# Kernel tuning notes

Hardware: AMD Instinct MI355X
Metric: run time of the kernel (lower is better)

Reference implementation:

```python
import math
import jax, jax.numpy as jnp
import numpy as np

B, T, D = 2, 2048, 1024
NUM_HEADS = 16
NUM_KV_HEADS = 4
HEAD_DIM = 64
ROPE_THETA = 500000.0


def precompute_freqs_cis(dim, seq_len, theta):
    freqs = 1.0 / theta ** (jnp.arange(0, dim, 2).astype(jnp.float32) / dim)
    freqs = jnp.outer(jnp.arange(seq_len), freqs)  # [T, dim//2]
    return jnp.cos(freqs), jnp.sin(freqs)


def apply_rotary_emb(xq, xk, cos, sin):
    # xq:[B,T,H,Dh], cos/sin:[T,Dh//2] -> broadcast as [1,T,1,Dh//2]
    c = cos[None, :, None, :]
    s = sin[None, :, None, :]

    def rot(x):
        xr = x.reshape(*x.shape[:-1], -1, 2)
        x0, x1 = xr[..., 0], xr[..., 1]
        return jnp.stack([x0 * c - x1 * s, x1 * c + x0 * s], axis=-1).reshape(x.shape)

    return rot(xq), rot(xk)


def setup_inputs() -> dict:
    key = jax.random.key(0)
    ks = jax.random.split(key, 5)
    x = jax.random.normal(ks[0], (B, T, D), dtype=jnp.float32)
    # causal mask [B,1,T,T]
    mask = jnp.broadcast_to(jnp.tril(jnp.ones((T, T), dtype=bool))[None, None], (B, 1, T, T))
    sq = 1.0 / math.sqrt(D)
    Wq = jax.random.normal(ks[1], (D, NUM_HEADS * HEAD_DIM), dtype=jnp.float32) * sq
    Wk = jax.random.normal(ks[2], (D, NUM_KV_HEADS * HEAD_DIM), dtype=jnp.float32) * sq
    Wv = jax.random.normal(ks[3], (D, NUM_KV_HEADS * HEAD_DIM), dtype=jnp.float32) * sq
    Wo = jax.random.normal(ks[4], (NUM_HEADS * HEAD_DIM, D), dtype=jnp.float32) * (1.0 / math.sqrt(NUM_HEADS * HEAD_DIM))
    return {"x": x, "mask": mask, "Wq": Wq, "Wk": Wk, "Wv": Wv, "Wo": Wo}


def reference(x, mask, Wq, Wk, Wv, Wo):
    b, t, _ = x.shape
    n_rep = NUM_HEADS // NUM_KV_HEADS
    q = (x @ Wq).reshape(b, t, NUM_HEADS, HEAD_DIM)
    k = (x @ Wk).reshape(b, t, NUM_KV_HEADS, HEAD_DIM)
    v = (x @ Wv).reshape(b, t, NUM_KV_HEADS, HEAD_DIM)
    cos, sin = precompute_freqs_cis(HEAD_DIM, t, ROPE_THETA)
    q, k = apply_rotary_emb(q, k, cos, sin)
    k = jnp.repeat(k, n_rep, axis=2)
    v = jnp.repeat(v, n_rep, axis=2)
    q = q.transpose(0, 2, 1, 3)  # [B,H,T,Dh]
    k = k.transpose(0, 2, 1, 3)
    v = v.transpose(0, 2, 1, 3)
    scale = 1.0 / math.sqrt(HEAD_DIM)
    attn = jnp.einsum('bhqd,bhkd->bhqk', q, k) * scale
    attn = jnp.where(mask, attn, -1e9)
    attn = jax.nn.softmax(attn, axis=-1)
    out = jnp.einsum('bhqk,bhkd->bhqd', attn, v)
    out = out.transpose(0, 2, 1, 3).reshape(b, t, -1)
    return out @ Wo
```

## Files before the change

### kernel.cpp

```cpp
#include <hip/hip_runtime.h>
#include <hip/hip_bf16.h>

#define B_  2
#define T_  2048
#define D_  1024
#define H_  16
#define KH_ 4
#define DH_ 64

typedef __attribute__((ext_vector_type(8))) short bf16x8;
typedef __attribute__((ext_vector_type(4))) float f32x4;

#define QSCALE 0.18033688011112043f

#if defined(__has_builtin)
#  if __has_builtin(__builtin_amdgcn_exp2f)
#    define EXP2F(x) __builtin_amdgcn_exp2f(x)
#  endif
#endif
#ifndef EXP2F
#  define EXP2F(x) exp2f(x)
#endif

__device__ __forceinline__ unsigned short f2bf(float f) {
  union { float f; unsigned int u; } v; v.f = f;
  return (unsigned short)((v.u + 0x7FFFu + ((v.u >> 16) & 1u)) >> 16);
}
__device__ __forceinline__ unsigned int pk2(float a, float b) {
  union { __hip_bfloat162 h2; unsigned int u; } v;
  v.h2 = __float22bfloat162_rn(make_float2(a, b));
  return v.u;
}

__device__ __forceinline__ void g2l16(const void* g, void* l) {
  __builtin_amdgcn_global_load_lds(
      (const __attribute__((address_space(1))) void*)g,
      (__attribute__((address_space(3))) void*)l, 16, 0, 0);
}


__global__ __launch_bounds__(256) void prep_kernel(
    const float* __restrict__ x,  const float* __restrict__ Wq,
    const float* __restrict__ Wk, const float* __restrict__ Wv,
    const float* __restrict__ Wo,
    short* __restrict__ xb, short* __restrict__ WT, short* __restrict__ WoT,
    float2* __restrict__ tbl) {
  __shared__ short Ts[64 * 72];
  const int bid = blockIdx.x, tid = threadIdx.x;

  if (bid < 2048) {
    const size_t i8 = ((size_t)bid * 256 + tid) * 8;
    const float4 a = *(const float4*)&x[i8];
    const float4 b = *(const float4*)&x[i8 + 4];
    uint4 p; p.x = pk2(a.x, a.y); p.y = pk2(a.z, a.w);
    p.z = pk2(b.x, b.y); p.w = pk2(b.z, b.w);
    *(uint4*)&xb[i8] = p;
  } else if (bid < 2688) {
    const bool isW = bid < 2432;
    const int idx = isW ? (bid - 2048) : (bid - 2432);
    const int n0 = (idx >> 4) * 64, k0 = (idx & 15) * 64;
    const float* src; int ncols, c0; short* dst;
    if (isW) {
      dst = WT;
      if (n0 < 1024)      { src = Wq; ncols = 1024; c0 = n0; }
      else if (n0 < 1280) { src = Wk; ncols = 256;  c0 = n0 - 1024; }
      else                { src = Wv; ncols = 256;  c0 = n0 - 1280; }
    } else { dst = WoT; src = Wo; ncols = 1024; c0 = n0; }
    for (int i = tid; i < 1024; i += 256) {
      const int kr = i >> 4, c4 = (i & 15) << 2;
      const int kc = isW ? kr : ((kr & 15) * 4 + (kr >> 4));
      const float4 w = *(const float4*)&src[(size_t)(k0 + kr) * ncols + c0 + c4];
      Ts[(c4 + 0) * 72 + kc] = (short)f2bf(w.x);
      Ts[(c4 + 1) * 72 + kc] = (short)f2bf(w.y);
      Ts[(c4 + 2) * 72 + kc] = (short)f2bf(w.z);
      Ts[(c4 + 3) * 72 + kc] = (short)f2bf(w.w);
    }
    __syncthreads();
    for (int c = tid; c < 512; c += 256) {
      const int nr = c >> 3, c8 = (c & 7) * 8;
      *(bf16x8*)&dst[(size_t)(n0 + nr) * 1024 + k0 + c8] =
          *(const bf16x8*)&Ts[nr * 72 + c8];
    }
  } else {
    const int e = (bid - 2688) * 256 + tid;
    const int t = e >> 5, i2 = e & 31;
    const float freq = exp2f(-(float)(2 * i2) * (18.931568569324174f / 64.0f));
    float sn, cs; sincosf((float)t * freq, &sn, &cs);
    tbl[e] = make_float2(cs, sn);
  }
}

__global__ __launch_bounds__(256) void qkv_mfma_kernel(
    const short* __restrict__ xb, const short* __restrict__ WT,
    const float2* __restrict__ tbl,
    short* __restrict__ qo, short* __restrict__ ko, short* __restrict__ vt) {
  __shared__ short Xs[128 * 128];
  __shared__ short Wt[64 * 128];
  const int tid = threadIdx.x;
  const int lane = tid & 63, w = tid >> 6;
  const int lm = lane & 15, quad = lane >> 4;
  const int lr = lane >> 4;
  const int lb = lane & 15;
  const int m0 = blockIdx.x * 128;
  const int n0 = blockIdx.y * 64;

  f32x4 acc[2][4];
  #pragma unroll
  for (int sm = 0; sm < 2; ++sm)
    #pragma unroll
    for (int ct = 0; ct < 4; ++ct) acc[sm][ct] = (f32x4){0.f, 0.f, 0.f, 0.f};

  for (int kt = 0; kt < 8; ++kt) {
    __syncthreads();
    #pragma unroll
    for (int u = 0; u < 8; ++u) {
      const int r = (w * 8 + u) * 4 + lr;
      const int sb = lb ^ (r & 7);
      g2l16(&xb[(size_t)(m0 + r) * 1024 + kt * 128 + sb * 8],
            &Xs[(w * 8 + u) * 512]);
    }
    #pragma unroll
    for (int u = 0; u < 4; ++u) {
      const int r = (w * 4 + u) * 4 + lr;
      const int sb = lb ^ (r & 7);
      g2l16(&WT[(size_t)(n0 + r) * 1024 + kt * 128 + sb * 8],
            &Wt[(w * 4 + u) * 512]);
    }
    asm volatile("s_waitcnt vmcnt(0)" ::: "memory");
    __syncthreads();
    #pragma unroll
    for (int s = 0; s < 4; ++s) {
      bf16x8 bfr[4];
      #pragma unroll
      for (int ct = 0; ct < 4; ++ct)
        bfr[ct] = *(const bf16x8*)&Wt[(ct * 16 + lm) * 128 +
                                      (((s * 4 + quad) ^ (lm & 7)) << 3)];
      #pragma unroll
      for (int sm = 0; sm < 2; ++sm) {
        const bf16x8 a = *(const bf16x8*)&Xs[(w * 32 + sm * 16 + lm) * 128 +
                                             (((s * 4 + quad) ^ (lm & 7)) << 3)];
        #pragma unroll
        for (int ct = 0; ct < 4; ++ct)
          acc[sm][ct] =
              __builtin_amdgcn_mfma_f32_16x16x32_bf16(a, bfr[ct], acc[sm][ct], 0, 0, 0);
      }
    }
  }

  if (n0 < 1280) {
    const bool isQ = n0 < 1024;
    short* outp = isQ ? qo : ko;
    const int base = isQ ? n0 : n0 - 1024;
    const int nh = isQ ? H_ : KH_;
    const int hh = base >> 6;
    const float post = isQ ? QSCALE : 1.0f;
    #pragma unroll
    for (int sm = 0; sm < 2; ++sm)
      #pragma unroll
      for (int r = 0; r < 4; ++r) {
        const int row = m0 + w * 32 + sm * 16 + quad * 4 + r;
        const int b = row >> 11, t = row & 2047;
        float v4[4];
        #pragma unroll
        for (int ct = 0; ct < 4; ++ct) {
          float val = acc[sm][ct][r];
          const float other = __shfl_xor(val, 1);
          const int ci = ct * 16 + lm;
          const float2 cs = tbl[t * 32 + (ci >> 1)];
          val = ((ci & 1) == 0) ? (val * cs.x - other * cs.y)
                                : (val * cs.x + other * cs.y);
          v4[ct] = val * post;
        }
        uint2 st; st.x = pk2(v4[0], v4[1]); st.y = pk2(v4[2], v4[3]);
        *(uint2*)&outp[((size_t)(b * nh + hh) * T_ + t) * DH_ + lm * 4] = st;
      }
  } else {
    __syncthreads();
    #pragma unroll
    for (int sm = 0; sm < 2; ++sm)
      #pragma unroll
      for (int r = 0; r < 4; ++r)
        #pragma unroll
        for (int ct = 0; ct < 4; ++ct)
          Xs[(w * 32 + sm * 16 + quad * 4 + r) * 72 + ct * 16 + lm] =
              (short)f2bf(acc[sm][ct][r]);
    __syncthreads();
    const int kh = (n0 - 1280) >> 6;
    const int b = m0 >> 11, t0 = m0 & 2047;
    short* vb = vt + (size_t)(b * KH_ + kh) * DH_ * T_;
    for (int c = tid; c < 1024; c += 256) {
      const int d = c >> 4, c8 = (c & 15) * 8;
      short tmp[8];
      #pragma unroll
      for (int j = 0; j < 8; ++j) {
        const int s = c8 + j, sg = s & 63;
        const int tok = (s & 64) + ((sg & 3) << 4) + (sg >> 2);
        tmp[j] = Xs[tok * 72 + d];
      }
      *(bf16x8*)&vb[(size_t)d * T_ + t0 + c8] = *(bf16x8*)tmp;
    }
  }
}

__global__ __launch_bounds__(256) void attn_mfma_kernel(
    const short* __restrict__ q, const short* __restrict__ k,
    const short* __restrict__ vt, short* __restrict__ att) {
  __shared__ short Ks[128 * 72];
  __shared__ short Vts[64 * 136];
  __shared__ short Ps0[64 * 72];
  __shared__ short Ps1[64 * 72];

  const int bx = blockIdx.x;
  const int qt = 31 - (bx >> 5);
  const int hb = bx & 31;
  const int h = hb >> 1, b = hb & 1;
  const int kh = h >> 2;
  const int tid = threadIdx.x;
  const int lane = tid & 63, w = tid >> 6;
  const int lm = lane & 15, quad = lane >> 4;
  const int q0 = qt * 64;

  const short* qb = q + (size_t)(b * H_ + h) * T_ * DH_;
  const short* kb = k + (size_t)(b * KH_ + kh) * T_ * DH_;
  const short* vb = vt + (size_t)(b * KH_ + kh) * DH_ * T_;

  bf16x8 ones;
  #pragma unroll
  for (int i = 0; i < 8; ++i) ones[i] = (short)0x3F80;

  bf16x8 aq[2];
  #pragma unroll
  for (int s = 0; s < 2; ++s)
    aq[s] = *(const bf16x8*)&qb[(size_t)(q0 + w * 16 + lm) * 64 + s * 32 + quad * 8];

  bf16x8 pk[4], pv[4];
  #pragma unroll
  for (int u = 0; u < 4; ++u) {
    const int c = tid + u * 256;
    const int row = c >> 3, c8 = (c & 7) * 8;
    pk[u] = *(const bf16x8*)&kb[(size_t)row * 64 + c8];
    const int d = c >> 4, c16 = (c & 15) * 8;
    pv[u] = *(const bf16x8*)&vb[(size_t)d * T_ + c16];
  }

  f32x4 oacc[4], lacc;
  #pragma unroll
  for (int i = 0; i < 4; ++i) oacc[i] = (f32x4){0.f, 0.f, 0.f, 0.f};
  lacc = (f32x4){0.f, 0.f, 0.f, 0.f};

  auto step = [&](int j, bool diag, short* Ps) {
    f32x4 sacc[4];
    #pragma unroll
    for (int i = 0; i < 4; ++i) sacc[i] = (f32x4){0.f, 0.f, 0.f, 0.f};
    __builtin_amdgcn_s_setprio(1);
    #pragma unroll
    for (int s = 0; s < 2; ++s) {
      #pragma unroll
      for (int ct = 0; ct < 4; ++ct) {
        const bf16x8 bb =
            *(const bf16x8*)&Ks[(j * 64 + ct * 16 + lm) * 72 + s * 32 + quad * 8];
        sacc[ct] = __builtin_amdgcn_mfma_f32_16x16x32_bf16(aq[s], bb, sacc[ct], 0, 0, 0);
      }
    }
    __builtin_amdgcn_s_setprio(0);
    if (diag) {
      #pragma unroll
      for (int r = 0; r < 4; ++r) {
        const int qi = w * 16 + quad * 4 + r;
        float p[4];
        #pragma unroll
        for (int ct = 0; ct < 4; ++ct) {
          float pv2 = EXP2F(sacc[ct][r]);
          if ((ct * 16 + lm) > qi) pv2 = 0.f;
          p[ct] = pv2;
        }
        uint2 pw2; pw2.x = pk2(p[0], p[1]); pw2.y = pk2(p[2], p[3]);
        *(uint2*)&Ps[qi * 72 + lm * 4] = pw2;
      }
    } else {
      #pragma unroll
      for (int r = 0; r < 4; ++r) {
        const int qi = w * 16 + quad * 4 + r;
        uint2 pw2;
        pw2.x = pk2(EXP2F(sacc[0][r]), EXP2F(sacc[1][r]));
        pw2.y = pk2(EXP2F(sacc[2][r]), EXP2F(sacc[3][r]));
        *(uint2*)&Ps[qi * 72 + lm * 4] = pw2;
      }
    }
    __builtin_amdgcn_s_setprio(1);
    #pragma unroll
    for (int s = 0; s < 2; ++s) {
      const bf16x8 pa = *(const bf16x8*)&Ps[(w * 16 + lm) * 72 + s * 32 + quad * 8];
      lacc = __builtin_amdgcn_mfma_f32_16x16x32_bf16(pa, ones, lacc, 0, 0, 0);
      #pragma unroll
      for (int ct = 0; ct < 4; ++ct) {
        const bf16x8 vfr = *(const bf16x8*)&Vts[(ct * 16 + lm) * 136 +
                                                j * 64 + s * 32 + quad * 8];
        oacc[ct] = __builtin_amdgcn_mfma_f32_16x16x32_bf16(pa, vfr, oacc[ct], 0, 0, 0);
      }
    }
    __builtin_amdgcn_s_setprio(0);
  };

  auto stage = [&](int r2) {
    __syncthreads();
    #pragma unroll
    for (int u = 0; u < 4; ++u) {
      const int c = tid + u * 256;
      const int row = c >> 3, c8 = (c & 7) * 8;
      *(bf16x8*)&Ks[row * 72 + c8] = pk[u];
      const int d = c >> 4, c16 = (c & 15) * 8;
      *(bf16x8*)&Vts[d * 136 + c16] = pv[u];
    }
    __syncthreads();
    const int r2n = (r2 + 2 <= qt) ? (r2 + 2) : r2;
    #pragma unroll
    for (int u = 0; u < 4; ++u) {
      const int c = tid + u * 256;
      const int row = c >> 3, c8 = (c & 7) * 8;
      pk[u] = *(const bf16x8*)&kb[(size_t)(r2n * 64 + row) * 64 + c8];
      const int d = c >> 4, c16 = (c & 15) * 8;
      pv[u] = *(const bf16x8*)&vb[(size_t)d * T_ + r2n * 64 + c16];
    }
  };

  int r2 = 0;
  for (; r2 + 1 <= qt; r2 += 2) {
    stage(r2);
    step(0, false, Ps0);
    step(1, r2 + 1 == qt, Ps1);
  }
  if (r2 == qt) {
    stage(r2);
    step(0, true, Ps0);
  }

  #pragma unroll
  for (int r = 0; r < 4; ++r) {
    const int qrow = q0 + w * 16 + quad * 4 + r;
    const float inv = 1.f / lacc[r];
    uint2 st;
    st.x = pk2(oacc[0][r] * inv, oacc[1][r] * inv);
    st.y = pk2(oacc[2][r] * inv, oacc[3][r] * inv);
    *(uint2*)&att[((size_t)b * T_ + qrow) * 1024 + h * 64 + lm * 4] = st;
  }
}

__global__ __launch_bounds__(256) void outproj_mfma_kernel(
    const short* __restrict__ att, const short* __restrict__ WoT,
    float* __restrict__ out) {
  __shared__ short Xs[128 * 128];
  __shared__ short Wt[64 * 128];
  const int tid = threadIdx.x;
  const int lane = tid & 63, w = tid >> 6;
  const int lm = lane & 15, quad = lane >> 4;
  const int lr = lane >> 4;
  const int lb = lane & 15;
  const int m0 = blockIdx.x * 128;
  const int n0 = blockIdx.y * 64;

  f32x4 acc[2][4];
  #pragma unroll
  for (int sm = 0; sm < 2; ++sm)
    #pragma unroll
    for (int ct = 0; ct < 4; ++ct) acc[sm][ct] = (f32x4){0.f, 0.f, 0.f, 0.f};

  for (int kt = 0; kt < 8; ++kt) {
    __syncthreads();
    #pragma unroll
    for (int u = 0; u < 8; ++u) {
      const int r = (w * 8 + u) * 4 + lr;
      const int sb = lb ^ (r & 7);
      g2l16(&att[(size_t)(m0 + r) * 1024 + kt * 128 + sb * 8],
            &Xs[(w * 8 + u) * 512]);
    }
    #pragma unroll
    for (int u = 0; u < 4; ++u) {
      const int r = (w * 4 + u) * 4 + lr;
      const int sb = lb ^ (r & 7);
      g2l16(&WoT[(size_t)(n0 + r) * 1024 + kt * 128 + sb * 8],
            &Wt[(w * 4 + u) * 512]);
    }
    asm volatile("s_waitcnt vmcnt(0)" ::: "memory");
    __syncthreads();
    #pragma unroll
    for (int s = 0; s < 4; ++s) {
      bf16x8 bfr[4];
      #pragma unroll
      for (int ct = 0; ct < 4; ++ct)
        bfr[ct] = *(const bf16x8*)&Wt[(ct * 16 + lm) * 128 +
                                      (((s * 4 + quad) ^ (lm & 7)) << 3)];
      #pragma unroll
      for (int sm = 0; sm < 2; ++sm) {
        const bf16x8 a = *(const bf16x8*)&Xs[(w * 32 + sm * 16 + lm) * 128 +
                                             (((s * 4 + quad) ^ (lm & 7)) << 3)];
        #pragma unroll
        for (int ct = 0; ct < 4; ++ct)
          acc[sm][ct] =
              __builtin_amdgcn_mfma_f32_16x16x32_bf16(a, bfr[ct], acc[sm][ct], 0, 0, 0);
      }
    }
  }

  #pragma unroll
  for (int sm = 0; sm < 2; ++sm)
    #pragma unroll
    for (int r = 0; r < 4; ++r) {
      const int row = m0 + w * 32 + sm * 16 + quad * 4 + r;
      #pragma unroll
      for (int ct = 0; ct < 4; ++ct)
        out[(size_t)row * 1024 + n0 + ct * 16 + lm] = acc[sm][ct][r];
    }
}

extern "C" void kernel_launch(void* const* d_in, const int* in_sizes, int n_in,
                              void* d_out, int out_size, void* d_ws, size_t ws_size,
                              hipStream_t stream) {
  const float* x  = (const float*)d_in[0];
  const float* Wq = (const float*)d_in[2];
  const float* Wk = (const float*)d_in[3];
  const float* Wv = (const float*)d_in[4];
  const float* Wo = (const float*)d_in[5];
  float* out = (float*)d_out;

  short* xb   = (short*)d_ws;
  short* WT   = xb  + (size_t)4194304;
  short* WoT  = WT  + (size_t)1572864;
  short* qb   = WoT + (size_t)1048576;
  short* kb   = qb  + (size_t)4194304;
  short* vtb  = kb  + (size_t)1048576;
  short* attb = vtb + (size_t)1048576;
  float2* tbl = (float2*)(attb + (size_t)4194304);

  prep_kernel<<<dim3(2944), dim3(256), 0, stream>>>(
      x, Wq, Wk, Wv, Wo, xb, WT, WoT, tbl);
  qkv_mfma_kernel<<<dim3(32, 24), dim3(256), 0, stream>>>(xb, WT, tbl, qb, kb, vtb);
  attn_mfma_kernel<<<dim3(1024), dim3(256), 0, stream>>>(qb, kb, vtb, attb);
  outproj_mfma_kernel<<<dim3(32, 16), dim3(256), 0, stream>>>(attb, WoT, out);
}
```

Before: 174.8 us.

## Keep attention probabilities in registers via transposed S MFMA and permuted V layout

Computes S transposed (K as the A operand) so each lane already holds the P fragment it needs for the PV MFMA. This removes the Ps shared-memory round trip, and the V-transpose token permutation in the projection kernel is changed to match the new key ordering. It also skips fully masked MFMA tiles on the diagonal block per wave, remaps blocks so heads alternate long and short query tiles for load balance, and adds an occupancy hint to launch_bounds. The risks are higher register pressure and correctness that depends on the permutation matching the fragment layout.

```diff
diff --git a/kernel.cpp b/kernel.cpp
--- a/kernel.cpp
+++ b/kernel.cpp
@@ -194,7 +194,8 @@
       #pragma unroll
       for (int j = 0; j < 8; ++j) {
         const int s = c8 + j, sg = s & 63;
-        const int tok = (s & 64) + ((sg & 3) << 4) + (sg >> 2);
+        const int tok = (s & 64) | (sg & 35) | (((sg >> 2) & 1) << 4) |
+                        (((sg >> 3) & 3) << 2);
         tmp[j] = Xs[tok * 72 + d];
       }
       *(bf16x8*)&vb[(size_t)d * T_ + t0 + c8] = *(bf16x8*)tmp;
@@ -202,17 +203,16 @@
   }
 }
 
-__global__ __launch_bounds__(256) void attn_mfma_kernel(
+__global__ __launch_bounds__(256, 4) void attn_mfma_kernel(
     const short* __restrict__ q, const short* __restrict__ k,
     const short* __restrict__ vt, short* __restrict__ att) {
   __shared__ short Ks[128 * 72];
   __shared__ short Vts[64 * 136];
-  __shared__ short Ps0[64 * 72];
-  __shared__ short Ps1[64 * 72];
 
   const int bx = blockIdx.x;
-  const int qt = 31 - (bx >> 5);
-  const int hb = bx & 31;
+  const int jj = bx & 255, c2 = bx >> 8;
+  int qt = (c2 & 1) ? (jj >> 3) : (31 - (jj >> 3));
+  const int hb = (jj & 7) | (c2 << 3);
   const int h = hb >> 1, b = hb & 1;
   const int kh = h >> 2;
   const int tid = threadIdx.x;
@@ -248,55 +248,52 @@
   for (int i = 0; i < 4; ++i) oacc[i] = (f32x4){0.f, 0.f, 0.f, 0.f};
   lacc = (f32x4){0.f, 0.f, 0.f, 0.f};
 
-  auto step = [&](int j, bool diag, short* Ps) {
+  auto step = [&](int j, bool diag) {
     f32x4 sacc[4];
     #pragma unroll
     for (int i = 0; i < 4; ++i) sacc[i] = (f32x4){0.f, 0.f, 0.f, 0.f};
     __builtin_amdgcn_s_setprio(1);
     #pragma unroll
-    for (int s = 0; s < 2; ++s) {
+    for (int s2 = 0; s2 < 2; ++s2) {
       #pragma unroll
       for (int ct = 0; ct < 4; ++ct) {
+        if (diag && ct > w) continue;
         const bf16x8 bb =
-            *(const bf16x8*)&Ks[(j * 64 + ct * 16 + lm) * 72 + s * 32 + quad * 8];
-        sacc[ct] = __builtin_amdgcn_mfma_f32_16x16x32_bf16(aq[s], bb, sacc[ct], 0, 0, 0);
+            *(const bf16x8*)&Ks[(j * 64 + ct * 16 + lm) * 72 + s2 * 32 + quad * 8];
+        sacc[ct] = __builtin_amdgcn_mfma_f32_16x16x32_bf16(bb, aq[s2], sacc[ct], 0, 0, 0);
       }
     }
     __builtin_amdgcn_s_setprio(0);
-    if (diag) {
+    unsigned int pd[4][2];
+    #pragma unroll
+    for (int ct = 0; ct < 4; ++ct) {
+      float p[4];
       #pragma unroll
       for (int r = 0; r < 4; ++r) {
-        const int qi = w * 16 + quad * 4 + r;
-        float p[4];
-        #pragma unroll
-        for (int ct = 0; ct < 4; ++ct) {
-          float pv2 = EXP2F(sacc[ct][r]);
-          if ((ct * 16 + lm) > qi) pv2 = 0.f;
-          p[ct] = pv2;
+        float e;
+        if (diag && ct > w) e = 0.f;
+        else {
+          e = EXP2F(sacc[ct][r]);
+          if (diag && ct == w && (quad * 4 + r) > lm) e = 0.f;
         }
-        uint2 pw2; pw2.x = pk2(p[0], p[1]); pw2.y = pk2(p[2], p[3]);
-        *(uint2*)&Ps[qi * 72 + lm * 4] = pw2;
-      }
-    } else {
-      #pragma unroll
-      for (int r = 0; r < 4; ++r) {
-        const int qi = w * 16 + quad * 4 + r;
-        uint2 pw2;
-        pw2.x = pk2(EXP2F(sacc[0][r]), EXP2F(sacc[1][r]));
-        pw2.y = pk2(EXP2F(sacc[2][r]), EXP2F(sacc[3][r]));
-        *(uint2*)&Ps[qi * 72 + lm * 4] = pw2;
-      }
+        p[r] = e;
+      }
+      pd[ct][0] = pk2(p[0], p[1]);
+      pd[ct][1] = pk2(p[2], p[3]);
     }
     __builtin_amdgcn_s_setprio(1);
     #pragma unroll
-    for (int s = 0; s < 2; ++s) {
-      const bf16x8 pa = *(const bf16x8*)&Ps[(w * 16 + lm) * 72 + s * 32 + quad * 8];
-      lacc = __builtin_amdgcn_mfma_f32_16x16x32_bf16(pa, ones, lacc, 0, 0, 0);
+    for (int s2 = 0; s2 < 2; ++s2) {
+      if (diag && 2 * s2 > w) continue;
+      union { bf16x8 v; unsigned int u[4]; } pa;
+      pa.u[0] = pd[2 * s2][0];     pa.u[1] = pd[2 * s2][1];
+      pa.u[2] = pd[2 * s2 + 1][0]; pa.u[3] = pd[2 * s2 + 1][1];
+      lacc = __builtin_amdgcn_mfma_f32_16x16x32_bf16(pa.v, ones, lacc, 0, 0, 0);
       #pragma unroll
       for (int ct = 0; ct < 4; ++ct) {
         const bf16x8 vfr = *(const bf16x8*)&Vts[(ct * 16 + lm) * 136 +
-                                                j * 64 + s * 32 + quad * 8];
-        oacc[ct] = __builtin_amdgcn_mfma_f32_16x16x32_bf16(pa, vfr, oacc[ct], 0, 0, 0);
+                                                j * 64 + s2 * 32 + quad * 8];
+        oacc[ct] = __builtin_amdgcn_mfma_f32_16x16x32_bf16(pa.v, vfr, oacc[ct], 0, 0, 0);
       }
     }
     __builtin_amdgcn_s_setprio(0);
@@ -327,12 +324,12 @@
   int r2 = 0;
   for (; r2 + 1 <= qt; r2 += 2) {
     stage(r2);
-    step(0, false, Ps0);
-    step(1, r2 + 1 == qt, Ps1);
+    step(0, false);
+    step(1, r2 + 1 == qt);
   }
   if (r2 == qt) {
     stage(r2);
-    step(0, true, Ps0);
+    step(0, true);
   }
 
   #pragma unroll
```

Measured after the change: 169.6 us. 3.0% less time.
